# Kernel tuning notes

Hardware: AMD Instinct MI355X
Metric: run time of the kernel (lower is better)

## Reference

```python
import jax, jax.numpy as jnp
import numpy as np

TOP_K = 2  # num_experts_per_tok


def setup_inputs() -> dict:
    key = jax.random.key(0)
    k1, k2, k3, k4, k5 = jax.random.split(key, 5)
    T, H, E, I = 8192, 2048, 8, 1024
    s = 0.02
    return {
        "x": jax.random.normal(k1, (T, H), dtype=jnp.float32),
        "w_gate": jax.random.normal(k2, (E, H), dtype=jnp.float32) * s,
        "w1": jax.random.normal(k3, (E, I, H), dtype=jnp.float32) * s,  # gate_proj
        "w3": jax.random.normal(k4, (E, I, H), dtype=jnp.float32) * s,  # up_proj
        "w2": jax.random.normal(k5, (E, H, I), dtype=jnp.float32) * s,  # down_proj
    }


def reference(x, w_gate, w1, w3, w2):
    # Router: logits -> softmax -> top-k -> renormalize (vLLM FusedMoE default)
    logits = jnp.einsum("th,eh->te", x, w_gate)               # [T, E]
    probs = jax.nn.softmax(logits, axis=-1)
    top_vals, top_idx = jax.lax.top_k(probs, TOP_K)           # [T, K]
    top_vals = top_vals / jnp.sum(top_vals, axis=-1, keepdims=True)
    E = w_gate.shape[0]
    # Dense per-token combine weights [T, E]; zero for non-selected experts.
    combine = jnp.sum(jax.nn.one_hot(top_idx, E, dtype=x.dtype)
                      * top_vals[..., None], axis=1)          # [T, E]

    # Per-expert SwiGLU MLP, weighted combine. Loop over small fixed E.
    out = jnp.zeros_like(x)
    for e in range(E):
        h = jax.nn.silu(x @ w1[e].T) * (x @ w3[e].T)          # [T, I]
        out = out + combine[:, e:e + 1] * (h @ w2[e].T)       # [T, H]
    return out
```

## Files before the change

kernel.cpp:

```cpp
#include <hip/hip_runtime.h>
#include <cstdint>
#include <cstddef>

#define T_TOK 8192
#define HDIM  2048
#define NEXP  8
#define IDIM  1024
#define CAP   17408
#define NTILE (CAP / 128)
#define LTOK  16

typedef __attribute__((ext_vector_type(8))) __bf16 bf16x8;
typedef __attribute__((ext_vector_type(4))) __bf16 bf16x4;
typedef __attribute__((ext_vector_type(4))) float  f32x4;

#define GLDS16(g, l)                                                        \
  __builtin_amdgcn_global_load_lds(                                         \
      (__attribute__((address_space(1))) void*)(g),                         \
      (__attribute__((address_space(3))) void*)(l), 16, 0, 0)

__global__ __launch_bounds__(256) void cvt_k(const float* __restrict__ src,
                                             __bf16* __restrict__ dst, int n4) {
  int i = blockIdx.x * blockDim.x + threadIdx.x;
  int stride = gridDim.x * blockDim.x;
  for (; i < n4; i += stride) {
    float4 v = ((const float4*)src)[i];
    bf16x4 b;
    b[0] = (__bf16)v.x; b[1] = (__bf16)v.y; b[2] = (__bf16)v.z; b[3] = (__bf16)v.w;
    ((bf16x4*)dst)[i] = b;
  }
}

__global__ __launch_bounds__(256) void logits_k(
    const float* __restrict__ x, const float* __restrict__ wg,
    __bf16* __restrict__ xb, int* __restrict__ tok_idx,
    float* __restrict__ tok_w) {
  __shared__ float wgs[NEXP * HDIM];
  {
    const float4* wg4 = (const float4*)wg;
    float4* wgs4 = (float4*)wgs;
    for (int i = threadIdx.x; i < NEXP * HDIM / 4; i += 256) wgs4[i] = wg4[i];
  }
  __syncthreads();

  const int wid  = threadIdx.x >> 6;
  const int lane = threadIdx.x & 63;

  for (int ti = 0; ti < LTOK / 4; ++ti) {
    const int t = blockIdx.x * LTOK + wid * (LTOK / 4) + ti;
    const float4* x4 = (const float4*)(x + (size_t)t * HDIM);
    bf16x4* xb4 = (bf16x4*)(xb + (size_t)t * HDIM);

    double acc[NEXP];
#pragma unroll
    for (int e = 0; e < NEXP; ++e) acc[e] = 0.0;

#pragma unroll
    for (int j = 0; j < 8; ++j) {
      int idx = j * 64 + lane;
      float4 xv = x4[idx];
      bf16x4 b;
      b[0] = (__bf16)xv.x; b[1] = (__bf16)xv.y; b[2] = (__bf16)xv.z; b[3] = (__bf16)xv.w;
      xb4[idx] = b;
#pragma unroll
      for (int e = 0; e < NEXP; ++e) {
        float4 wv = ((const float4*)(wgs + e * HDIM))[idx];
        acc[e] += (double)xv.x * wv.x + (double)xv.y * wv.y +
                  (double)xv.z * wv.z + (double)xv.w * wv.w;
      }
    }
#pragma unroll
    for (int off = 32; off > 0; off >>= 1)
#pragma unroll
      for (int e = 0; e < NEXP; ++e) acc[e] += __shfl_xor(acc[e], off, 64);

    if (lane == 0) {
      int i0 = 0; double m0 = acc[0];
      for (int e = 1; e < NEXP; ++e) if (acc[e] > m0) { m0 = acc[e]; i0 = e; }
      int i1 = -1; double m1 = -1e300;
      for (int e = 0; e < NEXP; ++e)
        if (e != i0 && acc[e] > m1) { m1 = acc[e]; i1 = e; }
      double p0 = 1.0 / (1.0 + exp(m1 - m0));
      tok_idx[t * 2 + 0] = i0;  tok_idx[t * 2 + 1] = i1;
      tok_w[t * 2 + 0] = (float)p0;
      tok_w[t * 2 + 1] = (float)(1.0 - p0);
    }
  }
}

__global__ __launch_bounds__(256) void hist_k(const int* __restrict__ tok_idx,
                                              int* __restrict__ counts) {
  __shared__ int h[NEXP];
  if (threadIdx.x < NEXP) h[threadIdx.x] = 0;
  __syncthreads();
  int t = blockIdx.x * blockDim.x + threadIdx.x;
  atomicAdd(&h[tok_idx[t * 2 + 0]], 1);
  atomicAdd(&h[tok_idx[t * 2 + 1]], 1);
  __syncthreads();
  if (threadIdx.x < NEXP) atomicAdd(&counts[threadIdx.x], h[threadIdx.x]);
}

__global__ void offsets_k(const int* __restrict__ counts, int* __restrict__ offp,
                          int* __restrict__ ctr2) {
  if (threadIdx.x == 0) {
    int off = 0;
    for (int e = 0; e < NEXP; ++e) { offp[e] = off; off += (counts[e] + 127) & ~127; }
    offp[NEXP] = off;
  }
  if (threadIdx.x < NEXP) ctr2[threadIdx.x] = 0;
}

__global__ __launch_bounds__(256) void assign_k(
    const int* __restrict__ tok_idx, const float* __restrict__ tok_w,
    const int* __restrict__ offp, int* __restrict__ ctr2,
    int* __restrict__ btok, float* __restrict__ bw, int* __restrict__ pos_of) {
  __shared__ int lcnt[NEXP], lbase[NEXP];
  if (threadIdx.x < NEXP) lcnt[threadIdx.x] = 0;
  __syncthreads();
  const int t  = blockIdx.x * blockDim.x + threadIdx.x;
  const int e0 = tok_idx[t * 2 + 0];
  const int e1 = tok_idx[t * 2 + 1];
  const int r0 = atomicAdd(&lcnt[e0], 1);
  const int r1 = atomicAdd(&lcnt[e1], 1);
  __syncthreads();
  if (threadIdx.x < NEXP)
    lbase[threadIdx.x] = atomicAdd(&ctr2[threadIdx.x], lcnt[threadIdx.x]);
  __syncthreads();
  int p0 = offp[e0] + lbase[e0] + r0;
  int p1 = offp[e1] + lbase[e1] + r1;
  btok[p0] = t;  bw[p0] = tok_w[t * 2 + 0];  pos_of[t * 2 + 0] = p0;
  btok[p1] = t;  bw[p1] = tok_w[t * 2 + 1];  pos_of[t * 2 + 1] = p1;
}

__device__ __forceinline__ int tile_expert(const int* offp, int slot0) {
  if (slot0 >= offp[NEXP]) return -1;
  int e = 0;
#pragma unroll
  for (int i = 1; i < NEXP; ++i) if (offp[i] <= slot0) e = i;
  return e;
}

__global__ __launch_bounds__(256, 2) void gemm1_k(
    const __bf16* __restrict__ xb, const __bf16* __restrict__ w1b,
    const __bf16* __restrict__ w3b, __bf16* __restrict__ h,
    const int* __restrict__ btok, const int* __restrict__ counts,
    const int* __restrict__ offp) {
  const int mt    = blockIdx.y;
  const int slot0 = mt * 128;
  const int e     = tile_expert(offp, slot0);
  if (e < 0) return;
  const int cnt  = counts[e];
  const int base = offp[e];
  const int mrow = slot0 - base;
  const int it   = blockIdx.x;

  __shared__ __align__(16) __bf16 As [128 * 32];
  __shared__ __align__(16) __bf16 B1s[128 * 32];
  __shared__ __align__(16) __bf16 B3s[128 * 32];

  const int tid  = threadIdx.x;
  const int lane = tid & 63;
  const int wid  = tid >> 6;
  const int wy   = wid >> 1, wx = wid & 1;

  const int r0 = tid >> 2;
  const int c8 = (tid & 3) * 8;
  int ma = mrow + r0, mb = ma + 64;
  int toka = btok[base + (ma < cnt ? ma : cnt - 1)];
  int tokb = btok[base + (mb < cnt ? mb : cnt - 1)];
  const __bf16* pA0  = xb + (size_t)toka * HDIM + c8;
  const __bf16* pA1  = xb + (size_t)tokb * HDIM + c8;
  const __bf16* pB1a = w1b + ((size_t)e * IDIM + it * 128 + r0) * HDIM + c8;
  const __bf16* pB1b = pB1a + (size_t)64 * HDIM;
  const __bf16* pB3a = w3b + ((size_t)e * IDIM + it * 128 + r0) * HDIM + c8;
  const __bf16* pB3b = pB3a + (size_t)64 * HDIM;

  const int wbase = wid * 512;
  __bf16* lA0  = As  + wbase;  __bf16* lA1  = As  + 2048 + wbase;
  __bf16* lB1a = B1s + wbase;  __bf16* lB1b = B1s + 2048 + wbase;
  __bf16* lB3a = B3s + wbase;  __bf16* lB3b = B3s + 2048 + wbase;

  f32x4 accg[4][4] = {};
  f32x4 accu[4][4] = {};
  const int frow = lane & 15;
  const int fk   = (lane >> 4) * 8;

  for (int kt = 0; kt < HDIM / 32; ++kt) {
    GLDS16(pA0, lA0);   GLDS16(pA1, lA1);
    GLDS16(pB1a, lB1a); GLDS16(pB1b, lB1b);
    GLDS16(pB3a, lB3a); GLDS16(pB3b, lB3b);
    pA0 += 32; pA1 += 32; pB1a += 32; pB1b += 32; pB3a += 32; pB3b += 32;
    __syncthreads();

    bf16x8 af[4], bf1[4], bf3[4];
#pragma unroll
    for (int mf = 0; mf < 4; ++mf)
      af[mf] = *(const bf16x8*)&As[(wy * 64 + mf * 16 + frow) * 32 + fk];
#pragma unroll
    for (int nf = 0; nf < 4; ++nf) {
      bf1[nf] = *(const bf16x8*)&B1s[(wx * 64 + nf * 16 + frow) * 32 + fk];
      bf3[nf] = *(const bf16x8*)&B3s[(wx * 64 + nf * 16 + frow) * 32 + fk];
    }
#pragma unroll
    for (int mf = 0; mf < 4; ++mf)
#pragma unroll
      for (int nf = 0; nf < 4; ++nf) {
        accg[mf][nf] = __builtin_amdgcn_mfma_f32_16x16x32_bf16(af[mf], bf1[nf], accg[mf][nf], 0, 0, 0);
        accu[mf][nf] = __builtin_amdgcn_mfma_f32_16x16x32_bf16(af[mf], bf3[nf], accu[mf][nf], 0, 0, 0);
      }
    __syncthreads();
  }

  const int i0c = it * 128 + wx * 64;
#pragma unroll
  for (int mf = 0; mf < 4; ++mf) {
    const int sbase = slot0 + wy * 64 + mf * 16 + (lane >> 4) * 4;
#pragma unroll
    for (int nf = 0; nf < 4; ++nf) {
      const int ic = i0c + nf * 16 + (lane & 15);
#pragma unroll
      for (int ri = 0; ri < 4; ++ri) {
        int s = sbase + ri;
        if (s - base < cnt) {
          float g = accg[mf][nf][ri];
          float u = accu[mf][nf][ri];
          float sv = g / (1.0f + __expf(-g)) * u;
          h[(size_t)s * IDIM + ic] = (__bf16)sv;
        }
      }
    }
  }
}

__global__ __launch_bounds__(256) void gemm2_k(
    const __bf16* __restrict__ h, const __bf16* __restrict__ w2b,
    __bf16* __restrict__ y, const float* __restrict__ bw,
    const int* __restrict__ offp) {
  const int mt    = blockIdx.y;
  const int slot0 = mt * 128;
  const int e     = tile_expert(offp, slot0);
  if (e < 0) return;
  const int nt = blockIdx.x;

  __shared__ __align__(16) __bf16 As[128 * 32];
  __shared__ __align__(16) __bf16 Bs[128 * 32];

  const int tid  = threadIdx.x;
  const int lane = tid & 63;
  const int wid  = tid >> 6;
  const int wy   = wid >> 1, wx = wid & 1;

  const int r0 = tid >> 2;
  const int c8 = (tid & 3) * 8;
  const __bf16* pA0 = h + ((size_t)slot0 + r0) * IDIM + c8;
  const __bf16* pA1 = pA0 + (size_t)64 * IDIM;
  const __bf16* pB0 = w2b + ((size_t)e * HDIM + nt * 128 + r0) * IDIM + c8;
  const __bf16* pB1 = pB0 + (size_t)64 * IDIM;

  const int wbase = wid * 512;
  __bf16* lA0 = As + wbase;  __bf16* lA1 = As + 2048 + wbase;
  __bf16* lB0 = Bs + wbase;  __bf16* lB1 = Bs + 2048 + wbase;

  f32x4 acc[4][4] = {};
  const int frow = lane & 15;
  const int fk   = (lane >> 4) * 8;

  for (int kt = 0; kt < IDIM / 32; ++kt) {
    GLDS16(pA0, lA0); GLDS16(pA1, lA1);
    GLDS16(pB0, lB0); GLDS16(pB1, lB1);
    pA0 += 32; pA1 += 32; pB0 += 32; pB1 += 32;
    __syncthreads();

    bf16x8 af[4], bf[4];
#pragma unroll
    for (int mf = 0; mf < 4; ++mf)
      af[mf] = *(const bf16x8*)&As[(wy * 64 + mf * 16 + frow) * 32 + fk];
#pragma unroll
    for (int nf = 0; nf < 4; ++nf)
      bf[nf] = *(const bf16x8*)&Bs[(wx * 64 + nf * 16 + frow) * 32 + fk];
#pragma unroll
    for (int mf = 0; mf < 4; ++mf)
#pragma unroll
      for (int nf = 0; nf < 4; ++nf)
        acc[mf][nf] = __builtin_amdgcn_mfma_f32_16x16x32_bf16(af[mf], bf[nf], acc[mf][nf], 0, 0, 0);
    __syncthreads();
  }

  const int ncol = nt * 128 + wx * 64;
#pragma unroll
  for (int mf = 0; mf < 4; ++mf) {
    const int sbase = slot0 + wy * 64 + mf * 16 + (lane >> 4) * 4;
#pragma unroll
    for (int ri = 0; ri < 4; ++ri) {
      int s = sbase + ri;
      float w = bw[s];
#pragma unroll
      for (int nf = 0; nf < 4; ++nf) {
        int c = ncol + nf * 16 + (lane & 15);
        y[(size_t)s * HDIM + c] = (__bf16)(acc[mf][nf][ri] * w);
      }
    }
  }
}

__global__ __launch_bounds__(256) void combine_k(
    const __bf16* __restrict__ y, const int* __restrict__ pos_of,
    float* __restrict__ out) {
  const int t  = blockIdx.x;
  const int c8 = threadIdx.x * 8;
  const int p0 = pos_of[t * 2 + 0];
  const int p1 = pos_of[t * 2 + 1];
  bf16x8 a = *(const bf16x8*)&y[(size_t)p0 * HDIM + c8];
  bf16x8 b = *(const bf16x8*)&y[(size_t)p1 * HDIM + c8];
  float4 o0, o1;
  o0.x = (float)a[0] + (float)b[0];  o0.y = (float)a[1] + (float)b[1];
  o0.z = (float)a[2] + (float)b[2];  o0.w = (float)a[3] + (float)b[3];
  o1.x = (float)a[4] + (float)b[4];  o1.y = (float)a[5] + (float)b[5];
  o1.z = (float)a[6] + (float)b[6];  o1.w = (float)a[7] + (float)b[7];
  float* op = out + (size_t)t * HDIM + c8;
  *(float4*)op = o0;
  *(float4*)(op + 4) = o1;
}

extern "C" void kernel_launch(void* const* d_in, const int* in_sizes, int n_in,
                              void* d_out, int out_size, void* d_ws, size_t ws_size,
                              hipStream_t stream) {
  (void)in_sizes; (void)n_in; (void)out_size; (void)ws_size;
  const float* x  = (const float*)d_in[0];
  const float* wg = (const float*)d_in[1];
  const float* w1 = (const float*)d_in[2];
  const float* w3 = (const float*)d_in[3];
  const float* w2 = (const float*)d_in[4];
  float* out = (float*)d_out;

  char* ws = (char*)d_ws;
  size_t off = 0;
  auto alloc = [&](size_t bytes) -> char* {
    char* p = ws + off;
    off += (bytes + 255) & ~(size_t)255;
    return p;
  };
  __bf16* xb      = (__bf16*)alloc((size_t)T_TOK * HDIM * 2);
  __bf16* w1b     = (__bf16*)alloc((size_t)NEXP * IDIM * HDIM * 2);
  __bf16* w3b     = (__bf16*)alloc((size_t)NEXP * IDIM * HDIM * 2);
  __bf16* w2b     = (__bf16*)alloc((size_t)NEXP * HDIM * IDIM * 2);
  __bf16* h       = (__bf16*)alloc((size_t)CAP * IDIM * 2);
  __bf16* y       = (__bf16*)alloc((size_t)CAP * HDIM * 2);
  int*    btok    = (int*)alloc((size_t)CAP * 4);
  float*  bw      = (float*)alloc((size_t)CAP * 4);
  int*    pos_of  = (int*)alloc((size_t)T_TOK * 2 * 4);
  int*    tok_idx = (int*)alloc((size_t)T_TOK * 2 * 4);
  float*  tok_w   = (float*)alloc((size_t)T_TOK * 2 * 4);
  int*    counts  = (int*)alloc(256);
  int*    ctr2    = (int*)alloc(256);
  int*    offp    = (int*)alloc(256);

  hipMemsetAsync(counts, 0, 768, stream);

  const int n4w = NEXP * IDIM * HDIM / 4;
  cvt_k<<<2048, 256, 0, stream>>>(w1, w1b, n4w);
  cvt_k<<<2048, 256, 0, stream>>>(w3, w3b, n4w);
  cvt_k<<<2048, 256, 0, stream>>>(w2, w2b, n4w);

  logits_k<<<T_TOK / LTOK, 256, 0, stream>>>(x, wg, xb, tok_idx, tok_w);
  hist_k<<<T_TOK / 256, 256, 0, stream>>>(tok_idx, counts);
  offsets_k<<<1, 64, 0, stream>>>(counts, offp, ctr2);
  assign_k<<<T_TOK / 256, 256, 0, stream>>>(tok_idx, tok_w, offp, ctr2, btok, bw, pos_of);

  gemm1_k<<<dim3(IDIM / 128, NTILE), 256, 0, stream>>>(xb, w1b, w3b, h, btok, counts, offp);
  gemm2_k<<<dim3(HDIM / 128, NTILE), 256, 0, stream>>>(h, w2b, y, bw, offp);
  combine_k<<<T_TOK, 256, 0, stream>>>(y, pos_of, out);
}
```

Baseline: 720.5 us.

## Double-buffer LDS tiles in both MoE GEMM kernels to overlap loads with MFMA

```diff
diff --git a/kernel.cpp b/kernel.cpp
--- a/kernel.cpp
+++ b/kernel.cpp
@@ -154,9 +154,9 @@
   const int mrow = slot0 - base;
   const int it   = blockIdx.x;
 
-  __shared__ __align__(16) __bf16 As [128 * 32];
-  __shared__ __align__(16) __bf16 B1s[128 * 32];
-  __shared__ __align__(16) __bf16 B3s[128 * 32];
+  __shared__ __align__(16) __bf16 As [2][128 * 32];
+  __shared__ __align__(16) __bf16 B1s[2][128 * 32];
+  __shared__ __align__(16) __bf16 B3s[2][128 * 32];
 
   const int tid  = threadIdx.x;
   const int lane = tid & 63;
@@ -176,40 +176,58 @@
   const __bf16* pB3b = pB3a + (size_t)64 * HDIM;
 
   const int wbase = wid * 512;
-  __bf16* lA0  = As  + wbase;  __bf16* lA1  = As  + 2048 + wbase;
-  __bf16* lB1a = B1s + wbase;  __bf16* lB1b = B1s + 2048 + wbase;
-  __bf16* lB3a = B3s + wbase;  __bf16* lB3b = B3s + 2048 + wbase;
 
   f32x4 accg[4][4] = {};
   f32x4 accu[4][4] = {};
   const int frow = lane & 15;
   const int fk   = (lane >> 4) * 8;
 
-  for (int kt = 0; kt < HDIM / 32; ++kt) {
-    GLDS16(pA0, lA0);   GLDS16(pA1, lA1);
-    GLDS16(pB1a, lB1a); GLDS16(pB1b, lB1b);
-    GLDS16(pB3a, lB3a); GLDS16(pB3b, lB3b);
-    pA0 += 32; pA1 += 32; pB1a += 32; pB1b += 32; pB3a += 32; pB3b += 32;
+#define G1_STAGE(b)                                                          \
+  do {                                                                       \
+    GLDS16(pA0,  As[b] + wbase);  GLDS16(pA1,  As[b] + 2048 + wbase);        \
+    GLDS16(pB1a, B1s[b] + wbase); GLDS16(pB1b, B1s[b] + 2048 + wbase);       \
+    GLDS16(pB3a, B3s[b] + wbase); GLDS16(pB3b, B3s[b] + 2048 + wbase);       \
+    pA0 += 32; pA1 += 32; pB1a += 32; pB1b += 32; pB3a += 32; pB3b += 32;    \
+  } while (0)
+
+#define G1_COMPUTE(b)                                                        \
+  do {                                                                       \
+    bf16x8 af[4], bf1[4], bf3[4];                                            \
+    _Pragma("unroll")                                                        \
+    for (int mf = 0; mf < 4; ++mf)                                           \
+      af[mf] = *(const bf16x8*)&As[b][(wy * 64 + mf * 16 + frow) * 32 + fk]; \
+    _Pragma("unroll")                                                        \
+    for (int nf = 0; nf < 4; ++nf) {                                         \
+      bf1[nf] = *(const bf16x8*)&B1s[b][(wx * 64 + nf * 16 + frow) * 32 + fk]; \
+      bf3[nf] = *(const bf16x8*)&B3s[b][(wx * 64 + nf * 16 + frow) * 32 + fk]; \
+    }                                                                        \
+    _Pragma("unroll")                                                        \
+    for (int mf = 0; mf < 4; ++mf)                                           \
+      _Pragma("unroll")                                                      \
+      for (int nf = 0; nf < 4; ++nf) {                                       \
+        accg[mf][nf] = __builtin_amdgcn_mfma_f32_16x16x32_bf16(af[mf], bf1[nf], accg[mf][nf], 0, 0, 0); \
+        accu[mf][nf] = __builtin_amdgcn_mfma_f32_16x16x32_bf16(af[mf], bf3[nf], accu[mf][nf], 0, 0, 0); \
+      }                                                                      \
+  } while (0)
+
+  G1_STAGE(0);
+  __syncthreads();
+#pragma unroll 1
+  for (int t = 0; t < 31; ++t) {
+    G1_STAGE(1);
+    G1_COMPUTE(0);
     __syncthreads();
-
-    bf16x8 af[4], bf1[4], bf3[4];
-#pragma unroll
-    for (int mf = 0; mf < 4; ++mf)
-      af[mf] = *(const bf16x8*)&As[(wy * 64 + mf * 16 + frow) * 32 + fk];
-#pragma unroll
-    for (int nf = 0; nf < 4; ++nf) {
-      bf1[nf] = *(const bf16x8*)&B1s[(wx * 64 + nf * 16 + frow) * 32 + fk];
-      bf3[nf] = *(const bf16x8*)&B3s[(wx * 64 + nf * 16 + frow) * 32 + fk];
-    }
-#pragma unroll
-    for (int mf = 0; mf < 4; ++mf)
-#pragma unroll
-      for (int nf = 0; nf < 4; ++nf) {
-        accg[mf][nf] = __builtin_amdgcn_mfma_f32_16x16x32_bf16(af[mf], bf1[nf], accg[mf][nf], 0, 0, 0);
-        accu[mf][nf] = __builtin_amdgcn_mfma_f32_16x16x32_bf16(af[mf], bf3[nf], accu[mf][nf], 0, 0, 0);
-      }
+    G1_STAGE(0);
+    G1_COMPUTE(1);
     __syncthreads();
   }
+  G1_STAGE(1);
+  G1_COMPUTE(0);
+  __syncthreads();
+  G1_COMPUTE(1);
+
+#undef G1_STAGE
+#undef G1_COMPUTE
 
   const int i0c = it * 128 + wx * 64;
 #pragma unroll
@@ -242,8 +260,8 @@
   if (e < 0) return;
   const int nt = blockIdx.x;
 
-  __shared__ __align__(16) __bf16 As[128 * 32];
-  __shared__ __align__(16) __bf16 Bs[128 * 32];
+  __shared__ __align__(16) __bf16 As[2][128 * 32];
+  __shared__ __align__(16) __bf16 Bs[2][128 * 32];
 
   const int tid  = threadIdx.x;
   const int lane = tid & 63;
@@ -258,33 +276,52 @@
   const __bf16* pB1 = pB0 + (size_t)64 * IDIM;
 
   const int wbase = wid * 512;
-  __bf16* lA0 = As + wbase;  __bf16* lA1 = As + 2048 + wbase;
-  __bf16* lB0 = Bs + wbase;  __bf16* lB1 = Bs + 2048 + wbase;
 
   f32x4 acc[4][4] = {};
   const int frow = lane & 15;
   const int fk   = (lane >> 4) * 8;
 
-  for (int kt = 0; kt < IDIM / 32; ++kt) {
-    GLDS16(pA0, lA0); GLDS16(pA1, lA1);
-    GLDS16(pB0, lB0); GLDS16(pB1, lB1);
-    pA0 += 32; pA1 += 32; pB0 += 32; pB1 += 32;
+#define G2_STAGE(b)                                                          \
+  do {                                                                       \
+    GLDS16(pA0, As[b] + wbase); GLDS16(pA1, As[b] + 2048 + wbase);           \
+    GLDS16(pB0, Bs[b] + wbase); GLDS16(pB1, Bs[b] + 2048 + wbase);           \
+    pA0 += 32; pA1 += 32; pB0 += 32; pB1 += 32;                              \
+  } while (0)
+
+#define G2_COMPUTE(b)                                                        \
+  do {                                                                       \
+    bf16x8 af[4], bf[4];                                                     \
+    _Pragma("unroll")                                                        \
+    for (int mf = 0; mf < 4; ++mf)                                           \
+      af[mf] = *(const bf16x8*)&As[b][(wy * 64 + mf * 16 + frow) * 32 + fk]; \
+    _Pragma("unroll")                                                        \
+    for (int nf = 0; nf < 4; ++nf)                                           \
+      bf[nf] = *(const bf16x8*)&Bs[b][(wx * 64 + nf * 16 + frow) * 32 + fk]; \
+    _Pragma("unroll")                                                        \
+    for (int mf = 0; mf < 4; ++mf)                                           \
+      _Pragma("unroll")                                                      \
+      for (int nf = 0; nf < 4; ++nf)                                         \
+        acc[mf][nf] = __builtin_amdgcn_mfma_f32_16x16x32_bf16(af[mf], bf[nf], acc[mf][nf], 0, 0, 0); \
+  } while (0)
+
+  G2_STAGE(0);
+  __syncthreads();
+#pragma unroll 1
+  for (int t = 0; t < 15; ++t) {
+    G2_STAGE(1);
+    G2_COMPUTE(0);
     __syncthreads();
-
-    bf16x8 af[4], bf[4];
-#pragma unroll
-    for (int mf = 0; mf < 4; ++mf)
-      af[mf] = *(const bf16x8*)&As[(wy * 64 + mf * 16 + frow) * 32 + fk];
-#pragma unroll
-    for (int nf = 0; nf < 4; ++nf)
-      bf[nf] = *(const bf16x8*)&Bs[(wx * 64 + nf * 16 + frow) * 32 + fk];
-#pragma unroll
-    for (int mf = 0; mf < 4; ++mf)
-#pragma unroll
-      for (int nf = 0; nf < 4; ++nf)
-        acc[mf][nf] = __builtin_amdgcn_mfma_f32_16x16x32_bf16(af[mf], bf[nf], acc[mf][nf], 0, 0, 0);
+    G2_STAGE(0);
+    G2_COMPUTE(1);
     __syncthreads();
   }
+  G2_STAGE(1);
+  G2_COMPUTE(0);
+  __syncthreads();
+  G2_COMPUTE(1);
+
+#undef G2_STAGE
+#undef G2_COMPUTE
 
   const int ncol = nt * 128 + wx * 64;
 #pragma unroll
```

After: 821.6 us. +14.0%, slower.

## Move expert GEMMs to 256x256 tiles with ping-pong LDS pipeline and fused gate/up weights

Applied to the files above, without the earlier changes.

```diff
diff --git a/kernel.cpp b/kernel.cpp
--- a/kernel.cpp
+++ b/kernel.cpp
@@ -6,8 +6,8 @@
 #define HDIM  2048
 #define NEXP  8
 #define IDIM  1024
-#define CAP   17408
-#define NTILE (CAP / 128)
+#define CAP   18432
+#define NTILE (CAP / 256)
 #define LTOK  16
 
 typedef __attribute__((ext_vector_type(8))) __bf16 bf16x8;
@@ -28,6 +28,25 @@
     bf16x4 b;
     b[0] = (__bf16)v.x; b[1] = (__bf16)v.y; b[2] = (__bf16)v.z; b[3] = (__bf16)v.w;
     ((bf16x4*)dst)[i] = b;
+  }
+}
+
+__global__ __launch_bounds__(256) void cvt13_k(const float* __restrict__ src,
+                                               __bf16* __restrict__ dst,
+                                               int is_w3) {
+  const int n4 = NEXP * IDIM * (HDIM / 4);
+  int i = blockIdx.x * blockDim.x + threadIdx.x;
+  int stride = gridDim.x * blockDim.x;
+  for (; i < n4; i += stride) {
+    int e   = i >> 19;
+    int rem = i & 524287;
+    int r   = rem >> 9;
+    int c4  = rem & 511;
+    int wrow = ((r >> 4) << 5) + (r & 15) + (is_w3 << 4);
+    float4 v = ((const float4*)src)[i];
+    bf16x4 b;
+    b[0] = (__bf16)v.x; b[1] = (__bf16)v.y; b[2] = (__bf16)v.z; b[3] = (__bf16)v.w;
+    ((bf16x4*)dst)[((size_t)e * 2 * IDIM + wrow) * 512 + c4] = b;
   }
 }
 
@@ -104,7 +123,7 @@
                           int* __restrict__ ctr2) {
   if (threadIdx.x == 0) {
     int off = 0;
-    for (int e = 0; e < NEXP; ++e) { offp[e] = off; off += (counts[e] + 127) & ~127; }
+    for (int e = 0; e < NEXP; ++e) { offp[e] = off; off += (counts[e] + 255) & ~255; }
     offp[NEXP] = off;
   }
   if (threadIdx.x < NEXP) ctr2[threadIdx.x] = 0;
@@ -140,167 +159,224 @@
   return e;
 }
 
-__global__ __launch_bounds__(256, 2) void gemm1_k(
-    const __bf16* __restrict__ xb, const __bf16* __restrict__ w1b,
-    const __bf16* __restrict__ w3b, __bf16* __restrict__ h,
-    const int* __restrict__ btok, const int* __restrict__ counts,
-    const int* __restrict__ offp) {
+#define BAR __builtin_amdgcn_s_barrier()
+#define VMC(N) asm volatile("s_waitcnt vmcnt(" #N ")" ::: "memory")
+
+#define STG(P0, P1, LB)                                                       \
+  { GLDS16(P0, (LB) + tid * 8);                                               \
+    GLDS16(P1, (LB) + 4096 + tid * 8);                                        \
+    P0 += 64; P1 += 64; }
+
+#define LOADA(BUF, HA)                                                        \
+  { _Pragma("unroll") for (int mf = 0; mf < 4; ++mf)                          \
+    _Pragma("unroll") for (int ks = 0; ks < 2; ++ks)                          \
+      a[mf][ks] = *(const bf16x8*)&As[(BUF)*16384 + (HA)*8192 +               \
+                                      ((wy*4 + mf)*2 + ks)*512 + laneAe]; }
+
+#define LOADB(BUF, HB)                                                        \
+  { _Pragma("unroll") for (int nf = 0; nf < 2; ++nf)                          \
+    _Pragma("unroll") for (int ks = 0; ks < 2; ++ks)                          \
+      b[nf][ks] = *(const bf16x8*)&Bs[(BUF)*16384 + (HB)*8192 +               \
+                                      ((wx*2 + nf)*2 + ks)*512 + laneAe]; }
+
+#define MFMAQ(HA, HB)                                                         \
+  { __builtin_amdgcn_s_setprio(1);                                            \
+    _Pragma("unroll") for (int mf = 0; mf < 4; ++mf)                          \
+    _Pragma("unroll") for (int nf = 0; nf < 2; ++nf)                          \
+    _Pragma("unroll") for (int ks = 0; ks < 2; ++ks)                          \
+      acc[(HA)*4 + mf][(HB)*2 + nf] = __builtin_amdgcn_mfma_f32_16x16x32_bf16(\
+          a[mf][ks], b[nf][ks], acc[(HA)*4 + mf][(HB)*2 + nf], 0, 0, 0);      \
+    __builtin_amdgcn_s_setprio(0); }
+
+#define FULLTILE(BUF, TC, NTK)                                                \
+  {                                                   \
+    LOADA(BUF, 0); LOADB(BUF, 0);                                             \
+    if ((TC) + 1 < (NTK)) { STG(pB1a, pB1b, Bs + ((BUF)^1)*16384 + 8192); }   \
+    BAR; MFMAQ(0, 0); BAR;                                                    \
+                                                      \
+    LOADB(BUF, 1);                                                            \
+    if ((TC) + 1 < (NTK)) { STG(pA1a, pA1b, As + ((BUF)^1)*16384 + 8192); }   \
+    BAR; MFMAQ(0, 1); BAR;                                                    \
+                                                      \
+    LOADA(BUF, 1); LOADB(BUF, 0);                                             \
+    if ((TC) + 2 < (NTK)) { STG(pA0a, pA0b, As + (BUF)*16384); }              \
+    BAR; MFMAQ(1, 0); BAR;                                                    \
+                                                      \
+    LOADB(BUF, 1);                                                            \
+    if ((TC) + 2 < (NTK)) { STG(pB0a, pB0b, Bs + (BUF)*16384); }              \
+    BAR; MFMAQ(1, 1);                                                         \
+    if ((TC) + 2 < (NTK))      { VMC(4); }                                    \
+    else if ((TC) + 1 < (NTK)) { VMC(0); }                                    \
+    BAR; }
+
+
+__global__ __launch_bounds__(512, 2) void gemm1_k(
+    const __bf16* __restrict__ xb, const __bf16* __restrict__ wcat,
+    __bf16* __restrict__ h, const int* __restrict__ btok,
+    const int* __restrict__ counts, const int* __restrict__ offp) {
   const int mt    = blockIdx.y;
-  const int slot0 = mt * 128;
+  const int slot0 = mt * 256;
   const int e     = tile_expert(offp, slot0);
   if (e < 0) return;
   const int cnt  = counts[e];
   const int base = offp[e];
   const int mrow = slot0 - base;
-  const int it   = blockIdx.x;
-
-  __shared__ __align__(16) __bf16 As [128 * 32];
-  __shared__ __align__(16) __bf16 B1s[128 * 32];
-  __shared__ __align__(16) __bf16 B3s[128 * 32];
+  const int nt   = blockIdx.x;
+
+  __shared__ __align__(16) __bf16 As[32768];
+  __shared__ __align__(16) __bf16 Bs[32768];
 
   const int tid  = threadIdx.x;
   const int lane = tid & 63;
   const int wid  = tid >> 6;
-  const int wy   = wid >> 1, wx = wid & 1;
-
-  const int r0 = tid >> 2;
-  const int c8 = (tid & 3) * 8;
-  int ma = mrow + r0, mb = ma + 64;
-  int toka = btok[base + (ma < cnt ? ma : cnt - 1)];
-  int tokb = btok[base + (mb < cnt ? mb : cnt - 1)];
-  const __bf16* pA0  = xb + (size_t)toka * HDIM + c8;
-  const __bf16* pA1  = xb + (size_t)tokb * HDIM + c8;
-  const __bf16* pB1a = w1b + ((size_t)e * IDIM + it * 128 + r0) * HDIM + c8;
-  const __bf16* pB1b = pB1a + (size_t)64 * HDIM;
-  const __bf16* pB3a = w3b + ((size_t)e * IDIM + it * 128 + r0) * HDIM + c8;
-  const __bf16* pB3b = pB3a + (size_t)64 * HDIM;
-
-  const int wbase = wid * 512;
-  __bf16* lA0  = As  + wbase;  __bf16* lA1  = As  + 2048 + wbase;
-  __bf16* lB1a = B1s + wbase;  __bf16* lB1b = B1s + 2048 + wbase;
-  __bf16* lB3a = B3s + wbase;  __bf16* lB3b = B3s + 2048 + wbase;
-
-  f32x4 accg[4][4] = {};
-  f32x4 accu[4][4] = {};
+  const int wy   = wid >> 2;
+  const int wx   = wid & 3;
   const int frow = lane & 15;
-  const int fk   = (lane >> 4) * 8;
-
-  for (int kt = 0; kt < HDIM / 32; ++kt) {
-    GLDS16(pA0, lA0);   GLDS16(pA1, lA1);
-    GLDS16(pB1a, lB1a); GLDS16(pB1b, lB1b);
-    GLDS16(pB3a, lB3a); GLDS16(pB3b, lB3b);
-    pA0 += 32; pA1 += 32; pB1a += 32; pB1b += 32; pB3a += 32; pB3b += 32;
-    __syncthreads();
-
-    bf16x8 af[4], bf1[4], bf3[4];
-#pragma unroll
-    for (int mf = 0; mf < 4; ++mf)
-      af[mf] = *(const bf16x8*)&As[(wy * 64 + mf * 16 + frow) * 32 + fk];
-#pragma unroll
-    for (int nf = 0; nf < 4; ++nf) {
-      bf1[nf] = *(const bf16x8*)&B1s[(wx * 64 + nf * 16 + frow) * 32 + fk];
-      bf3[nf] = *(const bf16x8*)&B3s[(wx * 64 + nf * 16 + frow) * 32 + fk];
-    }
-#pragma unroll
-    for (int mf = 0; mf < 4; ++mf)
-#pragma unroll
-      for (int nf = 0; nf < 4; ++nf) {
-        accg[mf][nf] = __builtin_amdgcn_mfma_f32_16x16x32_bf16(af[mf], bf1[nf], accg[mf][nf], 0, 0, 0);
-        accu[mf][nf] = __builtin_amdgcn_mfma_f32_16x16x32_bf16(af[mf], bf3[nf], accu[mf][nf], 0, 0, 0);
-      }
-    __syncthreads();
-  }
-
-  const int i0c = it * 128 + wx * 64;
-#pragma unroll
-  for (int mf = 0; mf < 4; ++mf) {
-    const int sbase = slot0 + wy * 64 + mf * 16 + (lane >> 4) * 4;
-#pragma unroll
-    for (int nf = 0; nf < 4; ++nf) {
-      const int ic = i0c + nf * 16 + (lane & 15);
-#pragma unroll
-      for (int ri = 0; ri < 4; ++ri) {
-        int s = sbase + ri;
-        if (s - base < cnt) {
-          float g = accg[mf][nf][ri];
-          float u = accu[mf][nf][ri];
-          float sv = g / (1.0f + __expf(-g)) * u;
-          h[(size_t)s * IDIM + ic] = (__bf16)sv;
+  const int laneAe = frow * 32 + (((lane >> 4) * 8) ^ ((frow & 8) << 1));
+
+  int rowS[2], colE[2];
+#pragma unroll
+  for (int L = 0; L < 2; ++L) {
+    int q = L * 8192 + ((tid * 16) ^ (tid & 32));
+    rowS[L] = (q >> 11) * 16 + ((q >> 6) & 15);
+    colE[L] = ((q >> 10) & 1) * 32 + ((q & 63) >> 1);
+  }
+
+  const __bf16 *pA0a, *pA0b, *pA1a, *pA1b;
+  {
+    int m, tok;
+    m = mrow + rowS[0];       m = m < cnt ? m : cnt - 1; tok = btok[base + m];
+    pA0a = xb + (size_t)tok * HDIM + colE[0];
+    m = mrow + rowS[1];       m = m < cnt ? m : cnt - 1; tok = btok[base + m];
+    pA0b = xb + (size_t)tok * HDIM + colE[1];
+    m = mrow + 128 + rowS[0]; m = m < cnt ? m : cnt - 1; tok = btok[base + m];
+    pA1a = xb + (size_t)tok * HDIM + colE[0];
+    m = mrow + 128 + rowS[1]; m = m < cnt ? m : cnt - 1; tok = btok[base + m];
+    pA1b = xb + (size_t)tok * HDIM + colE[1];
+  }
+  const __bf16* Bb = wcat + ((size_t)e * 2 * IDIM + nt * 256) * HDIM;
+  const __bf16* pB0a = Bb + (size_t)rowS[0] * HDIM + colE[0];
+  const __bf16* pB0b = Bb + (size_t)rowS[1] * HDIM + colE[1];
+  const __bf16* pB1a = Bb + (size_t)(128 + rowS[0]) * HDIM + colE[0];
+  const __bf16* pB1b = Bb + (size_t)(128 + rowS[1]) * HDIM + colE[1];
+
+  f32x4 acc[8][4] = {};
+  bf16x8 a[4][2], b[2][2];
+
+  STG(pA0a, pA0b, As + 0);
+  STG(pA1a, pA1b, As + 8192);
+  STG(pB0a, pB0b, Bs + 0);
+  STG(pB1a, pB1b, Bs + 8192);
+  STG(pA0a, pA0b, As + 16384);
+  STG(pB0a, pB0b, Bs + 16384);
+  VMC(4);
+  BAR;
+
+#pragma unroll 1
+  for (int t = 0; t < HDIM / 64; t += 2) {
+    FULLTILE(0, t, HDIM / 64);
+    FULLTILE(1, t + 1, HDIM / 64);
+  }
+
+  const int l4 = (lane >> 4) * 4;
+#pragma unroll
+  for (int hA = 0; hA < 2; ++hA)
+#pragma unroll
+    for (int mf = 0; mf < 4; ++mf) {
+      const int srow = slot0 + hA * 128 + wy * 64 + mf * 16 + l4;
+#pragma unroll
+      for (int hB = 0; hB < 2; ++hB) {
+        const int ic = nt * 128 + hB * 64 + wx * 16 + frow;
+#pragma unroll
+        for (int ri = 0; ri < 4; ++ri) {
+          const int s = srow + ri;
+          if (s - base < cnt) {
+            float g = acc[hA * 4 + mf][hB * 2 + 0][ri];
+            float u = acc[hA * 4 + mf][hB * 2 + 1][ri];
+            float sv = g / (1.0f + __expf(-g)) * u;
+            h[(size_t)s * IDIM + ic] = (__bf16)sv;
+          }
         }
       }
     }
-  }
-}
-
-__global__ __launch_bounds__(256) void gemm2_k(
-    const __bf16* __restrict__ h, const __bf16* __restrict__ w2b,
+}
+
+__global__ __launch_bounds__(512, 2) void gemm2_k(
+    const __bf16* __restrict__ hin, const __bf16* __restrict__ w2b,
     __bf16* __restrict__ y, const float* __restrict__ bw,
     const int* __restrict__ offp) {
   const int mt    = blockIdx.y;
-  const int slot0 = mt * 128;
+  const int slot0 = mt * 256;
   const int e     = tile_expert(offp, slot0);
   if (e < 0) return;
   const int nt = blockIdx.x;
 
-  __shared__ __align__(16) __bf16 As[128 * 32];
-  __shared__ __align__(16) __bf16 Bs[128 * 32];
+  __shared__ __align__(16) __bf16 As[32768];
+  __shared__ __align__(16) __bf16 Bs[32768];
 
   const int tid  = threadIdx.x;
   const int lane = tid & 63;
   const int wid  = tid >> 6;
-  const int wy   = wid >> 1, wx = wid & 1;
-
-  const int r0 = tid >> 2;
-  const int c8 = (tid & 3) * 8;
-  const __bf16* pA0 = h + ((size_t)slot0 + r0) * IDIM + c8;
-  const __bf16* pA1 = pA0 + (size_t)64 * IDIM;
-  const __bf16* pB0 = w2b + ((size_t)e * HDIM + nt * 128 + r0) * IDIM + c8;
-  const __bf16* pB1 = pB0 + (size_t)64 * IDIM;
-
-  const int wbase = wid * 512;
-  __bf16* lA0 = As + wbase;  __bf16* lA1 = As + 2048 + wbase;
-  __bf16* lB0 = Bs + wbase;  __bf16* lB1 = Bs + 2048 + wbase;
-
-  f32x4 acc[4][4] = {};
+  const int wy   = wid >> 2;
+  const int wx   = wid & 3;
   const int frow = lane & 15;
-  const int fk   = (lane >> 4) * 8;
-
-  for (int kt = 0; kt < IDIM / 32; ++kt) {
-    GLDS16(pA0, lA0); GLDS16(pA1, lA1);
-    GLDS16(pB0, lB0); GLDS16(pB1, lB1);
-    pA0 += 32; pA1 += 32; pB0 += 32; pB1 += 32;
-    __syncthreads();
-
-    bf16x8 af[4], bf[4];
-#pragma unroll
-    for (int mf = 0; mf < 4; ++mf)
-      af[mf] = *(const bf16x8*)&As[(wy * 64 + mf * 16 + frow) * 32 + fk];
-#pragma unroll
-    for (int nf = 0; nf < 4; ++nf)
-      bf[nf] = *(const bf16x8*)&Bs[(wx * 64 + nf * 16 + frow) * 32 + fk];
-#pragma unroll
-    for (int mf = 0; mf < 4; ++mf)
-#pragma unroll
-      for (int nf = 0; nf < 4; ++nf)
-        acc[mf][nf] = __builtin_amdgcn_mfma_f32_16x16x32_bf16(af[mf], bf[nf], acc[mf][nf], 0, 0, 0);
-    __syncthreads();
-  }
-
-  const int ncol = nt * 128 + wx * 64;
-#pragma unroll
-  for (int mf = 0; mf < 4; ++mf) {
-    const int sbase = slot0 + wy * 64 + mf * 16 + (lane >> 4) * 4;
-#pragma unroll
-    for (int ri = 0; ri < 4; ++ri) {
-      int s = sbase + ri;
-      float w = bw[s];
-#pragma unroll
-      for (int nf = 0; nf < 4; ++nf) {
-        int c = ncol + nf * 16 + (lane & 15);
-        y[(size_t)s * HDIM + c] = (__bf16)(acc[mf][nf][ri] * w);
+  const int laneAe = frow * 32 + (((lane >> 4) * 8) ^ ((frow & 8) << 1));
+
+  int rowS[2], colE[2];
+#pragma unroll
+  for (int L = 0; L < 2; ++L) {
+    int q = L * 8192 + ((tid * 16) ^ (tid & 32));
+    rowS[L] = (q >> 11) * 16 + ((q >> 6) & 15);
+    colE[L] = ((q >> 10) & 1) * 32 + ((q & 63) >> 1);
+  }
+
+  const __bf16* pA0a = hin + (size_t)(slot0 + rowS[0]) * IDIM + colE[0];
+  const __bf16* pA0b = hin + (size_t)(slot0 + rowS[1]) * IDIM + colE[1];
+  const __bf16* pA1a = hin + (size_t)(slot0 + 128 + rowS[0]) * IDIM + colE[0];
+  const __bf16* pA1b = hin + (size_t)(slot0 + 128 + rowS[1]) * IDIM + colE[1];
+  const __bf16* Bb = w2b + ((size_t)e * HDIM + nt * 256) * IDIM;
+  const __bf16* pB0a = Bb + (size_t)rowS[0] * IDIM + colE[0];
+  const __bf16* pB0b = Bb + (size_t)rowS[1] * IDIM + colE[1];
+  const __bf16* pB1a = Bb + (size_t)(128 + rowS[0]) * IDIM + colE[0];
+  const __bf16* pB1b = Bb + (size_t)(128 + rowS[1]) * IDIM + colE[1];
+
+  f32x4 acc[8][4] = {};
+  bf16x8 a[4][2], b[2][2];
+
+  STG(pA0a, pA0b, As + 0);
+  STG(pA1a, pA1b, As + 8192);
+  STG(pB0a, pB0b, Bs + 0);
+  STG(pB1a, pB1b, Bs + 8192);
+  STG(pA0a, pA0b, As + 16384);
+  STG(pB0a, pB0b, Bs + 16384);
+  VMC(4);
+  BAR;
+
+#pragma unroll 1
+  for (int t = 0; t < IDIM / 64; t += 2) {
+    FULLTILE(0, t, IDIM / 64);
+    FULLTILE(1, t + 1, IDIM / 64);
+  }
+
+  const int l4 = (lane >> 4) * 4;
+#pragma unroll
+  for (int hA = 0; hA < 2; ++hA)
+#pragma unroll
+    for (int mf = 0; mf < 4; ++mf) {
+      const int srow = slot0 + hA * 128 + wy * 64 + mf * 16 + l4;
+#pragma unroll
+      for (int ri = 0; ri < 4; ++ri) {
+        const int s = srow + ri;
+        const float w = bw[s];
+#pragma unroll
+        for (int hB = 0; hB < 2; ++hB)
+#pragma unroll
+          for (int nf = 0; nf < 2; ++nf) {
+            const int c = nt * 256 + hB * 128 + wx * 32 + nf * 16 + frow;
+            y[(size_t)s * HDIM + c] = (__bf16)(acc[hA * 4 + mf][hB * 2 + nf][ri] * w);
+          }
       }
     }
-  }
 }
 
 __global__ __launch_bounds__(256) void combine_k(
@@ -341,11 +417,9 @@
     return p;
   };
   __bf16* xb      = (__bf16*)alloc((size_t)T_TOK * HDIM * 2);
-  __bf16* w1b     = (__bf16*)alloc((size_t)NEXP * IDIM * HDIM * 2);
-  __bf16* w3b     = (__bf16*)alloc((size_t)NEXP * IDIM * HDIM * 2);
+  __bf16* wcat    = (__bf16*)alloc((size_t)NEXP * 2 * IDIM * HDIM * 2);
   __bf16* w2b     = (__bf16*)alloc((size_t)NEXP * HDIM * IDIM * 2);
   __bf16* h       = (__bf16*)alloc((size_t)CAP * IDIM * 2);
-  __bf16* y       = (__bf16*)alloc((size_t)CAP * HDIM * 2);
   int*    btok    = (int*)alloc((size_t)CAP * 4);
   float*  bw      = (float*)alloc((size_t)CAP * 4);
   int*    pos_of  = (int*)alloc((size_t)T_TOK * 2 * 4);
@@ -354,12 +428,13 @@
   int*    counts  = (int*)alloc(256);
   int*    ctr2    = (int*)alloc(256);
   int*    offp    = (int*)alloc(256);
+  __bf16* y       = (__bf16*)ws;
 
   hipMemsetAsync(counts, 0, 768, stream);
 
   const int n4w = NEXP * IDIM * HDIM / 4;
-  cvt_k<<<2048, 256, 0, stream>>>(w1, w1b, n4w);
-  cvt_k<<<2048, 256, 0, stream>>>(w3, w3b, n4w);
+  cvt13_k<<<2048, 256, 0, stream>>>(w1, wcat, 0);
+  cvt13_k<<<2048, 256, 0, stream>>>(w3, wcat, 1);
   cvt_k<<<2048, 256, 0, stream>>>(w2, w2b, n4w);
 
   logits_k<<<T_TOK / LTOK, 256, 0, stream>>>(x, wg, xb, tok_idx, tok_w);
@@ -367,7 +442,7 @@
   offsets_k<<<1, 64, 0, stream>>>(counts, offp, ctr2);
   assign_k<<<T_TOK / 256, 256, 0, stream>>>(tok_idx, tok_w, offp, ctr2, btok, bw, pos_of);
 
-  gemm1_k<<<dim3(IDIM / 128, NTILE), 256, 0, stream>>>(xb, w1b, w3b, h, btok, counts, offp);
-  gemm2_k<<<dim3(HDIM / 128, NTILE), 256, 0, stream>>>(h, w2b, y, bw, offp);
+  gemm1_k<<<dim3(IDIM / 128, NTILE), 512, 0, stream>>>(xb, wcat, h, btok, counts, offp);
+  gemm2_k<<<dim3(HDIM / 256, NTILE), 512, 0, stream>>>(h, w2b, y, bw, offp);
   combine_k<<<T_TOK, 256, 0, stream>>>(y, pos_of, out);
 }
```

New measurement: 699.8 us. 2.9% less time.
